# Kernel tuning notes

Hardware: AMD Instinct MI355X
Metric: run time of the kernel (lower is better)

## Reference

```python
import jax, jax.numpy as jnp
import numpy as np

N = 4096   # nodes
G = 64     # graphs
MH = 128   # hidden multiplicity (0e and 1o)
MU = 64    # up multiplicity (0e and 1o)
NSP = 10   # num_species
EPS = 1e-5


def _forward(nfh, nfu, onehot, W_h0, W_h1, W_u0, W_u1, Wt_00, Wt_11, Wt_01, Wt_10,
             W_p0, b_p0, W_p1, Wsc0, Wsc1, ln_w0, ln_b0, ln_w1, W_s0, b_s0, W_s1, batch):
    n = nfh.shape[0]
    # unpack irreps layout: [0e scalars | 1o vectors flattened]
    h0 = nfh[:, :MH]                       # [N, MH]
    h1 = nfh[:, MH:].reshape(n, MH, 3)     # [N, MH, 3]
    u0 = nfu[:, :MU]
    u1 = nfu[:, MU:].reshape(n, MU, 3)
    inv_h = 1.0 / np.sqrt(MH)
    inv_u = 1.0 / np.sqrt(MU)
    # irrep-wise (block-diagonal) o3.Linear, e3nn fan-in normalization
    hp0 = (h0 @ W_h0) * inv_h
    hp1 = jnp.einsum('nui,uv->nvi', h1, W_h1) * inv_h
    up0 = (u0 @ W_u0) * inv_u
    up1 = jnp.einsum('nui,uv->nvi', u1, W_u1) * inv_u
    # SeparateWeightTensorProduct: fully-connected 'uvw' CG tensor product
    # paths to 0e (scalars + gates, 2*MH outputs): 0e x 0e and 1o x 1o (dot / sqrt3)
    inv_tp = 1.0 / np.sqrt(2.0 * MH * MU)   # component/path normalization (2 paths, fan MH*MU)
    xy00 = jnp.einsum('nu,nv->nuv', hp0, up0).reshape(n, MH * MU)
    xy11 = jnp.einsum('nui,nvi->nuv', hp1, up1).reshape(n, MH * MU)
    z0 = (xy00 @ Wt_00.reshape(MH * MU, 2 * MH)
          + (xy11 @ Wt_11.reshape(MH * MU, 2 * MH)) / np.sqrt(3.0)) * inv_tp  # [N, 2*MH]
    # paths to 1o: 0e x 1o and 1o x 0e (staged to control intermediate size)
    ta = jnp.einsum('nu,uvw->nvw', hp0, Wt_01)       # [N, MU, MH]
    z1a = jnp.einsum('nvw,nvi->nwi', ta, up1)
    tb = jnp.einsum('nv,uvw->nuw', up0, Wt_10)       # [N, MH, MH]
    z1b = jnp.einsum('nuw,nui->nwi', tb, hp1)
    z1 = (z1a + z1b) * inv_tp                        # [N, MH, 3]
    # Gate nonlinearity: silu on scalars, sigmoid gates multiply 1o features
    s = jax.nn.silu(z0[:, :MH])
    g = jax.nn.sigmoid(z0[:, MH:])
    v = z1 * g[:, :, None]
    # lin_post (biases on scalars only)
    p0 = (s @ W_p0) * inv_h + b_p0
    p1 = jnp.einsum('nui,uv->nvi', v, W_p1) * inv_h
    # self-connection: FullyConnectedTensorProduct(hidden, NSPx0e, out)
    inv_sc = 1.0 / np.sqrt(MH * NSP)
    sxy0 = jnp.einsum('nu,nv->nuv', h0, onehot).reshape(n, MH * NSP)
    y0 = p0 + (sxy0 @ Wsc0.reshape(MH * NSP, MH)) * inv_sc
    sxy1 = jnp.einsum('nui,nv->nuvi', h1, onehot).reshape(n, MH * NSP, 3)
    y1 = p1 + jnp.einsum('nki,kw->nwi', sxy1, Wsc1.reshape(MH * NSP, MH)) * inv_sc
    # e3LayerNorm: per-graph stats; mean-subtract scalars only, RMS-normalize per irrep
    ones = jnp.ones((n,), y0.dtype)
    cnt = jnp.maximum(jax.ops.segment_sum(ones, batch, num_segments=G), 1.0)[:, None]
    mean0 = (jax.ops.segment_sum(y0, batch, num_segments=G) / cnt).mean(axis=1)  # [G]
    f0 = y0 - mean0[batch][:, None]
    var0 = (jax.ops.segment_sum(f0 * f0, batch, num_segments=G) / cnt).mean(axis=1)
    f0 = f0 / (jnp.sqrt(var0)[batch][:, None] + EPS) * ln_w0 + ln_b0
    var1 = (jax.ops.segment_sum((y1 * y1).reshape(n, -1), batch, num_segments=G) / cnt).mean(axis=1)
    f1 = y1 / (jnp.sqrt(var1)[batch][:, None, None] + EPS) * ln_w1[None, :, None]
    # residual skip connection (o3.Linear with scalar bias)
    out0 = f0 + (h0 @ W_s0) * inv_h + b_s0
    out1 = f1 + jnp.einsum('nui,uv->nvi', h1, W_s1) * inv_h
    return jnp.concatenate([out0, out1.reshape(n, 3 * MH)], axis=1)  # [N, 512]


def setup_inputs() -> dict:
    key = jax.random.key(0)
    ks = jax.random.split(key, 20)
    f = lambda i, shape: jax.random.normal(ks[i], shape, dtype=jnp.float32)
    species = jax.random.randint(ks[0], (N,), 0, NSP)
    return {
        'node_feats_hidden': f(1, (N, 4 * MH)),
        'node_feats_up': f(2, (N, 4 * MU)),
        'node_one_hot': jax.nn.one_hot(species, NSP, dtype=jnp.float32),
        'batch': jnp.sort(jax.random.randint(ks[3], (N,), 0, G)),
        'W_h0': f(4, (MH, MH)), 'W_h1': f(5, (MH, MH)),
        'W_u0': f(6, (MU, MU)), 'W_u1': f(7, (MU, MU)),
        'Wt_00': f(8, (MH, MU, 2 * MH)), 'Wt_11': f(9, (MH, MU, 2 * MH)),
        'Wt_01': f(10, (MH, MU, MH)), 'Wt_10': f(11, (MH, MU, MH)),
        'W_p0': f(12, (MH, MH)), 'b_p0': jnp.zeros((MH,), jnp.float32), 'W_p1': f(13, (MH, MH)),
        'Wsc0': f(14, (MH, NSP, MH)), 'Wsc1': f(15, (MH, NSP, MH)),
        'ln_w0': jnp.ones((MH,), jnp.float32), 'ln_b0': jnp.zeros((MH,), jnp.float32),
        'ln_w1': jnp.ones((MH,), jnp.float32),
        'W_s0': f(16, (MH, MH)), 'b_s0': jnp.zeros((MH,), jnp.float32), 'W_s1': f(17, (MH, MH)),
    }


def reference(node_feats_hidden, node_feats_up, node_one_hot, batch, W_h0, W_h1, W_u0, W_u1,
              Wt_00, Wt_11, Wt_01, Wt_10, W_p0, b_p0, W_p1, Wsc0, Wsc1, ln_w0, ln_b0, ln_w1,
              W_s0, b_s0, W_s1):
    return _forward(node_feats_hidden, node_feats_up, node_one_hot, W_h0, W_h1, W_u0, W_u1,
                    Wt_00, Wt_11, Wt_01, Wt_10, W_p0, b_p0, W_p1, Wsc0, Wsc1,
                    ln_w0, ln_b0, ln_w1, W_s0, b_s0, W_s1, batch)
```

## Files before the change

### kernel.cpp

```cpp
#include <hip/hip_runtime.h>
#include <cstdint>
#include <cstddef>


typedef _Float16 half8 __attribute__((ext_vector_type(8)));
typedef _Float16 half4v __attribute__((ext_vector_type(4)));
typedef float f32x4 __attribute__((ext_vector_type(4)));

static constexpr float INV_H  = 0.08838834764831845f;
static constexpr float INV_U  = 0.125f;
static constexpr float INV_TP = 0.0078125f;
static constexpr float INV_SC = 0.02795084971874737f;
static constexpr float RSQRT3 = 0.5773502691896258f;
static constexpr float LN_EPS = 1e-5f;

static constexpr size_t OFF_BZ0 = 0;
static constexpr size_t OFF_BZ1 = OFF_BZ0 + 8388608;
static constexpr size_t OFF_WH0 = OFF_BZ1 + 4194304;
static constexpr size_t OFF_WH1 = OFF_WH0 + 32768;
static constexpr size_t OFF_WU0 = OFF_WH1 + 32768;
static constexpr size_t OFF_WU1 = OFF_WU0 + 8192;
static constexpr size_t OFF_WP0 = OFF_WU1 + 8192;
static constexpr size_t OFF_WP1 = OFF_WP0 + 32768;
static constexpr size_t OFF_WS0 = OFF_WP1 + 32768;
static constexpr size_t OFF_WS1 = OFF_WS0 + 32768;
static constexpr size_t OFF_H0F = OFF_WS1 + 32768;
static constexpr size_t OFF_H1F = OFF_H0F + 1048576;
static constexpr size_t OFF_U0F = OFF_H1F + 3145728;
static constexpr size_t OFF_U1F = OFF_U0F + 524288;
static constexpr size_t OFF_HP0 = OFF_U1F + 1572864;
static constexpr size_t OFF_HP1 = OFF_HP0 + 1048576;
static constexpr size_t OFF_UP0 = OFF_HP1 + 3145728;
static constexpr size_t OFF_UP1 = OFF_UP0 + 524288;
static constexpr size_t OFF_SF  = OFF_UP1 + 1572864;
static constexpr size_t OFF_VF  = OFF_SF + 1048576;
static constexpr size_t OFF_PZ0 = OFF_VF + 3145728;
static constexpr size_t OFF_PZ1 = OFF_PZ0 + 16777216;
static constexpr size_t OFF_Y0  = OFF_PZ1 + 12582912;
static constexpr size_t OFF_Y1  = OFF_Y0 + 2097152;
static constexpr size_t OFF_O0  = OFF_Y1 + 6291456;
static constexpr size_t OFF_O1  = OFF_O0 + 2097152;
static constexpr size_t OFF_SP  = OFF_O1 + 6291456;
static constexpr size_t OFF_ST  = OFF_SP + 16384;
static constexpr size_t WS_NEED = OFF_ST + 2048;

__global__ __launch_bounds__(256) void kconv(
    const float* __restrict__ nfh, const float* __restrict__ nfu,
    const float* __restrict__ onehot,
    const float* __restrict__ Wt00, const float* __restrict__ Wt11,
    const float* __restrict__ Wt01, const float* __restrict__ Wt10,
    const float* __restrict__ Wh0, const float* __restrict__ Wh1,
    const float* __restrict__ Wu0, const float* __restrict__ Wu1,
    const float* __restrict__ Wp0, const float* __restrict__ Wp1,
    const float* __restrict__ Ws0, const float* __restrict__ Ws1,
    char* __restrict__ ws)
{
  const int bid = blockIdx.x, t = threadIdx.x;
  if (bid < 768) {
    _Float16* dst;
    int u, nt = 0;
    const bool isz0 = bid < 512;
    if (isz0) { nt = bid >> 8; u = bid & 255; dst = (_Float16*)(ws + OFF_BZ0) + ((size_t)nt*256 + (size_t)u)*8192; }
    else      { u = bid - 512;               dst = (_Float16*)(ws + OFF_BZ1) + (size_t)u*8192; }
    for (int it = 0; it < 4; ++it) {
      int chunk = it*256 + t;
      int lane = chunk & 63, ch = chunk >> 6;
      int f = ch >> 1, c = ch & 1;
      int w = f*16 + (lane & 15);
      int v0 = c*32 + (lane >> 4)*8;
      half8 o;
      #pragma unroll
      for (int j = 0; j < 8; ++j) {
        float val;
        if (isz0) {
          if (u < 128) val = Wt00[(size_t)((u*64 + v0 + j)*256) + nt*128 + w];
          else         val = Wt11[(size_t)(((u-128)*64 + v0 + j)*256) + nt*128 + w] * RSQRT3;
        } else {
          if (u < 128) val = Wt01[(size_t)((u*64 + v0 + j)*128) + w];
          else         val = Wt10[(size_t)(((u-128)*64 + v0 + j)*128) + w];
        }
        o[j] = (_Float16)val;
      }
      *(half8*)(dst + (size_t)chunk*8) = o;
    }
  } else if (bid < 776) {
    int mat = bid - 768;
    const float* src; size_t doff; int K, N;
    switch (mat) {
      case 0: src = Wh0; doff = OFF_WH0; K = 128; N = 128; break;
      case 1: src = Wh1; doff = OFF_WH1; K = 128; N = 128; break;
      case 2: src = Wu0; doff = OFF_WU0; K = 64;  N = 64;  break;
      case 3: src = Wu1; doff = OFF_WU1; K = 64;  N = 64;  break;
      case 4: src = Wp0; doff = OFF_WP0; K = 128; N = 128; break;
      case 5: src = Wp1; doff = OFF_WP1; K = 128; N = 128; break;
      case 6: src = Ws0; doff = OFF_WS0; K = 128; N = 128; break;
      default: src = Ws1; doff = OFF_WS1; K = 128; N = 128; break;
    }
    _Float16* d = (_Float16*)(ws + doff);
    const int nfr = N >> 4;
    const int chunks = (K*N) >> 3;
    for (int qd = t; qd < chunks; qd += 256) {
      int lane = qd & 63, cf = qd >> 6;
      int f = cf % nfr, c = cf / nfr;
      int col = f*16 + (lane & 15);
      int k0 = c*32 + (lane >> 4)*8;
      half8 o;
      #pragma unroll
      for (int j = 0; j < 8; ++j) o[j] = (_Float16)src[(size_t)(k0 + j)*N + col];
      *(half8*)(d + (size_t)qd*8) = o;
    }
  } else if (bid < 1544) {
    const int stride = 768*256;
    const int base = (bid - 776)*256 + t;
    _Float16* h0f = (_Float16*)(ws + OFF_H0F);
    _Float16* h1f = (_Float16*)(ws + OFF_H1F);
    _Float16* u0f = (_Float16*)(ws + OFF_U0F);
    _Float16* u1f = (_Float16*)(ws + OFF_U1F);
    for (int id = base; id < 524288; id += stride)
      h0f[id] = (_Float16)nfh[(size_t)(id >> 7)*512 + (id & 127)];
    for (int id = base; id < 1572864; id += stride) {
      int i = id >> 19, r = id & 524287, n = r >> 7, u = r & 127;
      h1f[id] = (_Float16)nfh[(size_t)n*512 + 128 + u*3 + i];
    }
    for (int id = base; id < 262144; id += stride)
      u0f[id] = (_Float16)nfu[(size_t)(id >> 6)*256 + (id & 63)];
    for (int id = base; id < 786432; id += stride) {
      int i = id >> 18, r = id & 262143, n = r >> 6, v = r & 63;
      u1f[id] = (_Float16)nfu[(size_t)n*256 + 64 + v*3 + i];
    }
  } else {
    int node = (bid - 1544)*256 + t;
    const float* row = onehot + (size_t)node*10;
    int best = 0; float bv = row[0];
    #pragma unroll
    for (int s = 1; s < 10; ++s) { float v = row[s]; if (v > bv) { bv = v; best = s; } }
    ((int*)(ws + OFF_SP))[node] = best;
  }
}

template<int KK, int NO, int MODE>
__global__ __launch_bounds__(256) void kgemm_small(char* __restrict__ ws,
    const float* __restrict__ bp0, const float* __restrict__ bs0)
{
  constexpr int NT = NO / 16;
  const int bid = blockIdx.x, t = threadIdx.x;
  const int lane = t & 63, wid = t >> 6;
  const int quad = lane >> 4, l15 = lane & 15;
  const int job = bid >> 5, n0 = (bid & 31) << 7;

  const _Float16 *A, *W;
  _Float16* oh = nullptr; float* of = nullptr;
  const float* bias = nullptr;
  float scale;
  if constexpr (MODE == 0) {
    scale = INV_H;
    if (job == 0) { A = (const _Float16*)(ws + OFF_H0F); W = (const _Float16*)(ws + OFF_WH0); oh = (_Float16*)(ws + OFF_HP0); }
    else {
      A = (const _Float16*)(ws + OFF_H1F) + (size_t)(job-1)*524288;
      W = (const _Float16*)(ws + OFF_WH1);
      oh = (_Float16*)(ws + OFF_HP1) + (size_t)(job-1)*524288;
    }
  } else if constexpr (MODE == 1) {
    scale = INV_U;
    if (job == 0) { A = (const _Float16*)(ws + OFF_U0F); W = (const _Float16*)(ws + OFF_WU0); oh = (_Float16*)(ws + OFF_UP0); }
    else {
      A = (const _Float16*)(ws + OFF_U1F) + (size_t)(job-1)*262144;
      W = (const _Float16*)(ws + OFF_WU1);
      oh = (_Float16*)(ws + OFF_UP1) + (size_t)(job-1)*262144;
    }
  } else {
    scale = INV_H;
    switch (job) {
      case 0: A = (const _Float16*)(ws + OFF_SF);  W = (const _Float16*)(ws + OFF_WP0); of = (float*)(ws + OFF_Y0); bias = bp0; break;
      case 1: A = (const _Float16*)(ws + OFF_H0F); W = (const _Float16*)(ws + OFF_WS0); of = (float*)(ws + OFF_O0); bias = bs0; break;
      case 2: case 3: case 4:
        A = (const _Float16*)(ws + OFF_VF) + (size_t)(job-2)*524288;
        W = (const _Float16*)(ws + OFF_WP1);
        of = (float*)(ws + OFF_Y1) + (size_t)(job-2)*524288; break;
      default:
        A = (const _Float16*)(ws + OFF_H1F) + (size_t)(job-5)*524288;
        W = (const _Float16*)(ws + OFF_WS1);
        of = (float*)(ws + OFF_O1) + (size_t)(job-5)*524288; break;
    }
  }

  f32x4 acc[2][NT];
  const f32x4 zz = {0.f, 0.f, 0.f, 0.f};
  #pragma unroll
  for (int mf = 0; mf < 2; ++mf)
    #pragma unroll
    for (int nf = 0; nf < NT; ++nf) acc[mf][nf] = zz;

  #pragma unroll
  for (int kc = 0; kc < KK/32; ++kc) {
    half8 a[2];
    #pragma unroll
    for (int mf = 0; mf < 2; ++mf)
      a[mf] = *(const half8*)(A + (size_t)(n0 + wid*32 + mf*16 + l15)*KK + kc*32 + quad*8);
    #pragma unroll
    for (int nf = 0; nf < NT; ++nf) {
      half8 b = *(const half8*)(W + (size_t)(kc*NT + nf)*512 + lane*8);
      #pragma unroll
      for (int mf = 0; mf < 2; ++mf)
        acc[mf][nf] = __builtin_amdgcn_mfma_f32_16x16x32_f16(a[mf], b, acc[mf][nf], 0, 0, 0);
    }
  }

  #pragma unroll
  for (int mf = 0; mf < 2; ++mf)
    #pragma unroll
    for (int nf = 0; nf < NT; ++nf) {
      int col = nf*16 + l15;
      float bv = bias ? bias[col] : 0.f;
      #pragma unroll
      for (int r = 0; r < 4; ++r) {
        int row = n0 + wid*32 + mf*16 + quad*4 + r;
        float v = acc[mf][nf][r] * scale + bv;
        if constexpr (MODE < 2) oh[(size_t)row*NO + col] = (_Float16)v;
        else                    of[(size_t)row*NO + col] = v;
      }
    }
}

__global__ __launch_bounds__(256, 2) void kbig(char* __restrict__ ws)
{
  const int bid = blockIdx.x, t = threadIdx.x;
  const int lane = t & 63, wid = t >> 6;
  const int wy = wid >> 1, wx = wid & 1;
  const int quad = lane >> 4, l15 = lane & 15;

  const _Float16* hp0 = (const _Float16*)(ws + OFF_HP0);
  const _Float16* hp1 = (const _Float16*)(ws + OFF_HP1);
  const _Float16* up0 = (const _Float16*)(ws + OFF_UP0);
  const _Float16* up1 = (const _Float16*)(ws + OFF_UP1);

  const _Float16 *p, *q, *B0;
  float* out; int opitch; size_t obase; int node0;
  if (bid < 256) {
    int mt = bid >> 3, nt = (bid >> 2) & 1, kj = bid & 3;
    node0 = mt << 7;
    if (kj == 0) { p = hp0; q = up0; }
    else { p = hp1 + (size_t)(kj-1)*524288; q = up1 + (size_t)(kj-1)*262144; }
    B0 = (const _Float16*)(ws + OFF_BZ0) + (size_t)nt*2097152 + (kj ? (size_t)1048576 : (size_t)0);
    out = (float*)(ws + OFF_PZ0) + (size_t)kj*1048576;
    obase = (size_t)node0*256 + (size_t)nt*128;
    opitch = 256;
  } else {
    int b2 = bid - 256, mt = b2 >> 1, kj = b2 & 1, i = mt >> 5;
    node0 = (mt & 31) << 7;
    if (kj == 0) { p = hp0; q = up1 + (size_t)i*262144; }
    else         { p = hp1 + (size_t)i*524288; q = up0; }
    B0 = (const _Float16*)(ws + OFF_BZ1) + (kj ? (size_t)1048576 : (size_t)0);
    out = (float*)(ws + OFF_PZ1) + (size_t)kj*1572864;
    obase = (size_t)mt*16384;
    opitch = 128;
  }

  half8 qf[4][2];
  #pragma unroll
  for (int mf = 0; mf < 4; ++mf)
    #pragma unroll
    for (int c = 0; c < 2; ++c)
      qf[mf][c] = *(const half8*)(q + (size_t)(node0 + wy*64 + mf*16 + l15)*64 + c*32 + quad*8);

  f32x4 acc[4][4];
  const f32x4 zz = {0.f, 0.f, 0.f, 0.f};
  #pragma unroll
  for (int mf = 0; mf < 4; ++mf)
    #pragma unroll
    for (int nf = 0; nf < 4; ++nf) acc[mf][nf] = zz;

  const _Float16* prow = p + (size_t)(node0 + wy*64 + l15)*128;
  const _Float16* Bw = B0 + (size_t)wx*4096 + (size_t)lane*8;

  for (int u4 = 0; u4 < 32; ++u4) {
    half4v pw[4];
    #pragma unroll
    for (int mf = 0; mf < 4; ++mf)
      pw[mf] = *(const half4v*)(prow + (size_t)mf*2048 + u4*4);
    #pragma unroll
    for (int uu = 0; uu < 4; ++uu) {
      const _Float16* Bu = Bw + (size_t)(u4*4 + uu)*8192;
      half8 bf[2][4];
      #pragma unroll
      for (int c = 0; c < 2; ++c)
        #pragma unroll
        for (int nf = 0; nf < 4; ++nf)
          bf[c][nf] = *(const half8*)(Bu + (size_t)((nf*2 + c)*512));
      #pragma unroll
      for (int mf = 0; mf < 4; ++mf) {
        const _Float16 ps = pw[mf][uu];
        const half8 pv = {ps, ps, ps, ps, ps, ps, ps, ps};
        #pragma unroll
        for (int c = 0; c < 2; ++c) {
          half8 a = qf[mf][c] * pv;
          #pragma unroll
          for (int nf = 0; nf < 4; ++nf)
            acc[mf][nf] = __builtin_amdgcn_mfma_f32_16x16x32_f16(a, bf[c][nf], acc[mf][nf], 0, 0, 0);
        }
      }
    }
  }

  #pragma unroll
  for (int mf = 0; mf < 4; ++mf)
    #pragma unroll
    for (int nf = 0; nf < 4; ++nf) {
      int col = wx*64 + nf*16 + l15;
      #pragma unroll
      for (int r = 0; r < 4; ++r) {
        int row = wy*64 + mf*16 + quad*4 + r;
        out[obase + (size_t)row*opitch + col] = acc[mf][nf][r];
      }
    }
}

__global__ __launch_bounds__(256) void kreduce(char* __restrict__ ws)
{
  const int id = blockIdx.x*256 + threadIdx.x;
  const int n = id >> 7, w = id & 127;
  const float* pz0 = (const float*)(ws + OFF_PZ0);
  const float* pz1 = (const float*)(ws + OFF_PZ1);
  _Float16* sf = (_Float16*)(ws + OFF_SF);
  _Float16* vf = (_Float16*)(ws + OFF_VF);
  const size_t b = (size_t)n*256;
  float zs = (pz0[b + w] + pz0[1048576 + b + w] + pz0[2097152 + b + w] + pz0[3145728 + b + w]) * INV_TP;
  float zg = (pz0[b + 128 + w] + pz0[1048576 + b + 128 + w] + pz0[2097152 + b + 128 + w] + pz0[3145728 + b + 128 + w]) * INV_TP;
  float s = zs / (1.f + __expf(-zs));
  float g = 1.f / (1.f + __expf(-zg));
  sf[id] = (_Float16)s;
  #pragma unroll
  for (int i = 0; i < 3; ++i) {
    size_t r = ((size_t)i*4096 + (size_t)n)*128 + w;
    float z1v = (pz1[r] + pz1[1572864 + r]) * INV_TP;
    vf[(size_t)i*524288 + (size_t)n*128 + w] = (_Float16)(z1v * g);
  }
}

__global__ __launch_bounds__(256) void ksc(char* __restrict__ ws,
    const float* __restrict__ nfh,
    const float* __restrict__ Wsc0, const float* __restrict__ Wsc1)
{
  const int t = threadIdx.x;
  const int node = blockIdx.x*2 + (t >> 7);
  const int w = t & 127;
  const int sp = ((const int*)(ws + OFF_SP))[node];
  const float* h = nfh + (size_t)node*512;
  float a0 = 0.f, a10 = 0.f, a11 = 0.f, a12 = 0.f;
  for (int u = 0; u < 128; ++u) {
    const size_t wi = (size_t)(u*10 + sp)*128 + w;
    float w0 = Wsc0[wi];
    float w1 = Wsc1[wi];
    a0 += h[u] * w0;
    a10 += h[128 + u*3 + 0] * w1;
    a11 += h[128 + u*3 + 1] * w1;
    a12 += h[128 + u*3 + 2] * w1;
  }
  float* y0 = (float*)(ws + OFF_Y0);
  float* y1 = (float*)(ws + OFF_Y1);
  y0[(size_t)node*128 + w] += INV_SC * a0;
  y1[(size_t)node*128 + w] += INV_SC * a10;
  y1[524288 + (size_t)node*128 + w] += INV_SC * a11;
  y1[1048576 + (size_t)node*128 + w] += INV_SC * a12;
}

__global__ __launch_bounds__(256) void kstats1(char* __restrict__ ws, const int* __restrict__ batch)
{
  const int t = threadIdx.x;
  const int node = blockIdx.x*32 + (t >> 3);
  const int sub = t & 7;
  const float* y0 = (const float*)(ws + OFF_Y0) + (size_t)node*128;
  const float* y1 = (const float*)(ws + OFF_Y1);
  float s0 = 0.f, ss0 = 0.f, ss1 = 0.f;
  for (int c = sub*16; c < sub*16 + 16; ++c) { float v = y0[c]; s0 += v; ss0 += v*v; }
  #pragma unroll
  for (int i = 0; i < 3; ++i) {
    const float* yp = y1 + (size_t)i*524288 + (size_t)node*128;
    for (int c = sub*16; c < sub*16 + 16; ++c) { float v = yp[c]; ss1 += v*v; }
  }
  #pragma unroll
  for (int m = 1; m < 8; m <<= 1) {
    s0  += __shfl_xor(s0, m, 64);
    ss0 += __shfl_xor(ss0, m, 64);
    ss1 += __shfl_xor(ss1, m, 64);
  }
  if (sub == 0) {
    float* st = (float*)(ws + OFF_ST);
    int g = batch[node];
    atomicAdd(&st[g], s0);
    atomicAdd(&st[64 + g], ss0);
    atomicAdd(&st[128 + g], ss1);
    atomicAdd(&st[192 + g], 1.f);
  }
}

__global__ void kstats2(char* __restrict__ ws)
{
  const int g = threadIdx.x;
  if (g >= 64) return;
  float* st = (float*)(ws + OFF_ST);
  float c = fmaxf(st[192 + g], 1.f);
  float m0 = st[g] / (c * 128.f);
  float var0 = st[64 + g] / (c * 128.f) - m0*m0;
  float var1 = st[128 + g] / (c * 384.f);
  st[256 + g] = m0;
  st[320 + g] = 1.f / (sqrtf(fmaxf(var0, 0.f)) + LN_EPS);
  st[384 + g] = 1.f / (sqrtf(fmaxf(var1, 0.f)) + LN_EPS);
}

__global__ __launch_bounds__(256) void kfinal(char* __restrict__ ws, const int* __restrict__ batch,
    const float* __restrict__ lnw0, const float* __restrict__ lnb0, const float* __restrict__ lnw1,
    float* __restrict__ outp)
{
  const int id = blockIdx.x*256 + threadIdx.x;
  const int n = id >> 9, c = id & 511;
  const float* st = (const float*)(ws + OFF_ST);
  const int g = batch[n];
  float val;
  if (c < 128) {
    const float* y0 = (const float*)(ws + OFF_Y0);
    const float* o0 = (const float*)(ws + OFF_O0);
    val = (y0[(size_t)n*128 + c] - st[256 + g]) * st[320 + g] * lnw0[c] + lnb0[c] + o0[(size_t)n*128 + c];
  } else {
    int cc = c - 128, w = cc / 3, i = cc - w*3;
    const float* y1 = (const float*)(ws + OFF_Y1);
    const float* o1 = (const float*)(ws + OFF_O1);
    val = y1[(size_t)i*524288 + (size_t)n*128 + w] * st[384 + g] * lnw1[w]
        + o1[(size_t)i*524288 + (size_t)n*128 + w];
  }
  outp[id] = val;
}

extern "C" void kernel_launch(void* const* d_in, const int* in_sizes, int n_in,
                              void* d_out, int out_size, void* d_ws, size_t ws_size,
                              hipStream_t stream)
{
  const float* nfh   = (const float*)d_in[0];
  const float* nfu   = (const float*)d_in[1];
  const float* oneh  = (const float*)d_in[2];
  const int*   batch = (const int*)d_in[3];
  const float* Wh0   = (const float*)d_in[4];
  const float* Wh1   = (const float*)d_in[5];
  const float* Wu0   = (const float*)d_in[6];
  const float* Wu1   = (const float*)d_in[7];
  const float* Wt00  = (const float*)d_in[8];
  const float* Wt11  = (const float*)d_in[9];
  const float* Wt01  = (const float*)d_in[10];
  const float* Wt10  = (const float*)d_in[11];
  const float* Wp0   = (const float*)d_in[12];
  const float* bp0   = (const float*)d_in[13];
  const float* Wp1   = (const float*)d_in[14];
  const float* Wsc0  = (const float*)d_in[15];
  const float* Wsc1  = (const float*)d_in[16];
  const float* lnw0  = (const float*)d_in[17];
  const float* lnb0  = (const float*)d_in[18];
  const float* lnw1  = (const float*)d_in[19];
  const float* Ws0   = (const float*)d_in[20];
  const float* bs0   = (const float*)d_in[21];
  const float* Ws1   = (const float*)d_in[22];
  char* ws = (char*)d_ws;

  if (ws_size < WS_NEED) {
    hipMemsetAsync(d_out, 0, (size_t)out_size * sizeof(float), stream);
    return;
  }

  hipMemsetAsync(ws + OFF_ST, 0, 2048, stream);
  kconv<<<1560, 256, 0, stream>>>(nfh, nfu, oneh, Wt00, Wt11, Wt01, Wt10,
                                  Wh0, Wh1, Wu0, Wu1, Wp0, Wp1, Ws0, Ws1, ws);
  kgemm_small<128,128,0><<<128, 256, 0, stream>>>(ws, nullptr, nullptr);
  kgemm_small<64, 64, 1><<<128, 256, 0, stream>>>(ws, nullptr, nullptr);
  kbig<<<448, 256, 0, stream>>>(ws);
  kreduce<<<2048, 256, 0, stream>>>(ws);
  kgemm_small<128,128,2><<<256, 256, 0, stream>>>(ws, bp0, bs0);
  ksc<<<2048, 256, 0, stream>>>(ws, nfh, Wsc0, Wsc1);
  kstats1<<<128, 256, 0, stream>>>(ws, batch);
  kstats2<<<1, 64, 0, stream>>>(ws);
  kfinal<<<8192, 256, 0, stream>>>(ws, batch, lnw0, lnb0, lnw1, (float*)d_out);
}
```

Baseline: 367.4 us.

## Fuse stats into self-connection, drop memset and stats2, double-buffer B loads in kbig

Several changes at once. The stats accumulator is zeroed inside kconv instead of by a separate memset. The self-connection kernel now also computes the per-graph sums with wave and block reductions, which removes the kstats1 re-read of y0/y1 and the kstats2 launch, and kfinal now derives mean and inverse std per element itself. The big GEMM loop software-pipelines the B fragment and p loads with two register buffers so loads overlap the MFMAs. The cost is higher register pressure in kbig and redundant sqrt/div work per element in kfinal.

```diff
diff --git a/kernel.cpp b/kernel.cpp
--- a/kernel.cpp
+++ b/kernel.cpp
@@ -135,6 +135,10 @@
     #pragma unroll
     for (int s = 1; s < 10; ++s) { float v = row[s]; if (v > bv) { bv = v; best = s; } }
     ((int*)(ws + OFF_SP))[node] = best;
+    if (bid == 1544) {
+      float* stz = (float*)(ws + OFF_ST);
+      stz[t] = 0.f; stz[t + 256] = 0.f;
+    }
   }
 }
 
@@ -273,33 +277,55 @@
   const _Float16* prow = p + (size_t)(node0 + wy*64 + l15)*128;
   const _Float16* Bw = B0 + (size_t)wx*4096 + (size_t)lane*8;
 
-  for (int u4 = 0; u4 < 32; ++u4) {
-    half4v pw[4];
-    #pragma unroll
-    for (int mf = 0; mf < 4; ++mf)
-      pw[mf] = *(const half4v*)(prow + (size_t)mf*2048 + u4*4);
-    #pragma unroll
-    for (int uu = 0; uu < 4; ++uu) {
-      const _Float16* Bu = Bw + (size_t)(u4*4 + uu)*8192;
-      half8 bf[2][4];
-      #pragma unroll
-      for (int c = 0; c < 2; ++c)
+  auto loadB = [&](half8 (&dst)[2][4], int uidx) {
+    const _Float16* Bu = Bw + (size_t)uidx*8192;
+    #pragma unroll
+    for (int c = 0; c < 2; ++c)
+      #pragma unroll
+      for (int nf = 0; nf < 4; ++nf)
+        dst[c][nf] = *(const half8*)(Bu + (size_t)((nf*2 + c)*512));
+  };
+  auto mstep = [&](const half8 (&bf)[2][4], const half4v (&pwl)[4], int uu) {
+    #pragma unroll
+    for (int mf = 0; mf < 4; ++mf) {
+      const _Float16 ps = pwl[mf][uu];
+      const half8 pv = {ps, ps, ps, ps, ps, ps, ps, ps};
+      #pragma unroll
+      for (int c = 0; c < 2; ++c) {
+        half8 a = qf[mf][c] * pv;
         #pragma unroll
         for (int nf = 0; nf < 4; ++nf)
-          bf[c][nf] = *(const half8*)(Bu + (size_t)((nf*2 + c)*512));
-      #pragma unroll
-      for (int mf = 0; mf < 4; ++mf) {
-        const _Float16 ps = pw[mf][uu];
-        const half8 pv = {ps, ps, ps, ps, ps, ps, ps, ps};
-        #pragma unroll
-        for (int c = 0; c < 2; ++c) {
-          half8 a = qf[mf][c] * pv;
-          #pragma unroll
-          for (int nf = 0; nf < 4; ++nf)
-            acc[mf][nf] = __builtin_amdgcn_mfma_f32_16x16x32_f16(a, bf[c][nf], acc[mf][nf], 0, 0, 0);
-        }
+          acc[mf][nf] = __builtin_amdgcn_mfma_f32_16x16x32_f16(a, bf[c][nf], acc[mf][nf], 0, 0, 0);
       }
     }
+  };
+
+  half4v pw[4], pwN[4];
+  #pragma unroll
+  for (int mf = 0; mf < 4; ++mf)
+    pw[mf] = *(const half4v*)(prow + (size_t)mf*2048);
+
+  half8 bfA[2][4], bfB[2][4];
+  loadB(bfA, 0);
+
+  for (int u4 = 0; u4 < 32; ++u4) {
+    const int b = u4*4;
+    loadB(bfB, b + 1);
+    mstep(bfA, pw, 0);
+    loadB(bfA, b + 2);
+    mstep(bfB, pw, 1);
+    {
+      const int np = (u4 < 31) ? (u4 + 1)*4 : u4*4;
+      #pragma unroll
+      for (int mf = 0; mf < 4; ++mf)
+        pwN[mf] = *(const half4v*)(prow + (size_t)mf*2048 + np);
+    }
+    loadB(bfB, b + 3);
+    mstep(bfA, pw, 2);
+    loadB(bfA, (u4 < 31) ? (b + 4) : (b + 3));
+    mstep(bfB, pw, 3);
+    #pragma unroll
+    for (int mf = 0; mf < 4; ++mf) pw[mf] = pwN[mf];
   }
 
   #pragma unroll
@@ -337,9 +363,10 @@
   }
 }
 
-__global__ __launch_bounds__(256) void ksc(char* __restrict__ ws,
+__global__ __launch_bounds__(256) void kscstats(char* __restrict__ ws,
     const float* __restrict__ nfh,
-    const float* __restrict__ Wsc0, const float* __restrict__ Wsc1)
+    const float* __restrict__ Wsc0, const float* __restrict__ Wsc1,
+    const int* __restrict__ batch)
 {
   const int t = threadIdx.x;
   const int node = blockIdx.x*2 + (t >> 7);
@@ -358,54 +385,37 @@
   }
   float* y0 = (float*)(ws + OFF_Y0);
   float* y1 = (float*)(ws + OFF_Y1);
-  y0[(size_t)node*128 + w] += INV_SC * a0;
-  y1[(size_t)node*128 + w] += INV_SC * a10;
-  y1[524288 + (size_t)node*128 + w] += INV_SC * a11;
-  y1[1048576 + (size_t)node*128 + w] += INV_SC * a12;
-}
-
-__global__ __launch_bounds__(256) void kstats1(char* __restrict__ ws, const int* __restrict__ batch)
-{
-  const int t = threadIdx.x;
-  const int node = blockIdx.x*32 + (t >> 3);
-  const int sub = t & 7;
-  const float* y0 = (const float*)(ws + OFF_Y0) + (size_t)node*128;
-  const float* y1 = (const float*)(ws + OFF_Y1);
-  float s0 = 0.f, ss0 = 0.f, ss1 = 0.f;
-  for (int c = sub*16; c < sub*16 + 16; ++c) { float v = y0[c]; s0 += v; ss0 += v*v; }
-  #pragma unroll
-  for (int i = 0; i < 3; ++i) {
-    const float* yp = y1 + (size_t)i*524288 + (size_t)node*128;
-    for (int c = sub*16; c < sub*16 + 16; ++c) { float v = yp[c]; ss1 += v*v; }
-  }
-  #pragma unroll
-  for (int m = 1; m < 8; m <<= 1) {
+  const size_t i0 = (size_t)node*128 + w;
+  float y0n  = y0[i0]           + INV_SC * a0;
+  float y1n0 = y1[i0]           + INV_SC * a10;
+  float y1n1 = y1[524288 + i0]  + INV_SC * a11;
+  float y1n2 = y1[1048576 + i0] + INV_SC * a12;
+  y0[i0] = y0n;
+  y1[i0] = y1n0;
+  y1[524288 + i0]  = y1n1;
+  y1[1048576 + i0] = y1n2;
+
+  float s0 = y0n, ss0 = y0n*y0n, ss1 = y1n0*y1n0 + y1n1*y1n1 + y1n2*y1n2;
+  #pragma unroll
+  for (int m = 1; m < 64; m <<= 1) {
     s0  += __shfl_xor(s0, m, 64);
     ss0 += __shfl_xor(ss0, m, 64);
     ss1 += __shfl_xor(ss1, m, 64);
   }
-  if (sub == 0) {
-    float* st = (float*)(ws + OFF_ST);
-    int g = batch[node];
-    atomicAdd(&st[g], s0);
-    atomicAdd(&st[64 + g], ss0);
-    atomicAdd(&st[128 + g], ss1);
-    atomicAdd(&st[192 + g], 1.f);
-  }
-}
-
-__global__ void kstats2(char* __restrict__ ws)
-{
-  const int g = threadIdx.x;
-  if (g >= 64) return;
-  float* st = (float*)(ws + OFF_ST);
-  float c = fmaxf(st[192 + g], 1.f);
-  float m0 = st[g] / (c * 128.f);
-  float var0 = st[64 + g] / (c * 128.f) - m0*m0;
-  float var1 = st[128 + g] / (c * 384.f);
-  st[256 + g] = m0;
-  st[320 + g] = 1.f / (sqrtf(fmaxf(var0, 0.f)) + LN_EPS);
-  st[384 + g] = 1.f / (sqrtf(fmaxf(var1, 0.f)) + LN_EPS);
+  __shared__ float red[4][3];
+  if ((t & 63) == 0) {
+    red[t >> 6][0] = s0; red[t >> 6][1] = ss0; red[t >> 6][2] = ss1;
+  }
+  __syncthreads();
+  if ((t & 127) == 0) {
+    const int wv = t >> 6;
+    float* stp = (float*)(ws + OFF_ST);
+    const int g = batch[node];
+    atomicAdd(&stp[g],       red[wv][0] + red[wv+1][0]);
+    atomicAdd(&stp[64 + g],  red[wv][1] + red[wv+1][1]);
+    atomicAdd(&stp[128 + g], red[wv][2] + red[wv+1][2]);
+    atomicAdd(&stp[192 + g], 1.f);
+  }
 }
 
 __global__ __launch_bounds__(256) void kfinal(char* __restrict__ ws, const int* __restrict__ batch,
@@ -416,16 +426,21 @@
   const int n = id >> 9, c = id & 511;
   const float* st = (const float*)(ws + OFF_ST);
   const int g = batch[n];
+  const float cnt = fmaxf(st[192 + g], 1.f);
   float val;
   if (c < 128) {
     const float* y0 = (const float*)(ws + OFF_Y0);
     const float* o0 = (const float*)(ws + OFF_O0);
-    val = (y0[(size_t)n*128 + c] - st[256 + g]) * st[320 + g] * lnw0[c] + lnb0[c] + o0[(size_t)n*128 + c];
+    float m0   = st[g] / (cnt * 128.f);
+    float var0 = st[64 + g] / (cnt * 128.f) - m0*m0;
+    float inv0 = 1.f / (sqrtf(fmaxf(var0, 0.f)) + LN_EPS);
+    val = (y0[(size_t)n*128 + c] - m0) * inv0 * lnw0[c] + lnb0[c] + o0[(size_t)n*128 + c];
   } else {
     int cc = c - 128, w = cc / 3, i = cc - w*3;
     const float* y1 = (const float*)(ws + OFF_Y1);
     const float* o1 = (const float*)(ws + OFF_O1);
-    val = y1[(size_t)i*524288 + (size_t)n*128 + w] * st[384 + g] * lnw1[w]
+    float inv1 = 1.f / (sqrtf(fmaxf(st[128 + g] / (cnt * 384.f), 0.f)) + LN_EPS);
+    val = y1[(size_t)i*524288 + (size_t)n*128 + w] * inv1 * lnw1[w]
         + o1[(size_t)i*524288 + (size_t)n*128 + w];
   }
   outp[id] = val;
@@ -465,7 +480,6 @@
     return;
   }
 
-  hipMemsetAsync(ws + OFF_ST, 0, 2048, stream);
   kconv<<<1560, 256, 0, stream>>>(nfh, nfu, oneh, Wt00, Wt11, Wt01, Wt10,
                                   Wh0, Wh1, Wu0, Wu1, Wp0, Wp1, Ws0, Ws1, ws);
   kgemm_small<128,128,0><<<128, 256, 0, stream>>>(ws, nullptr, nullptr);
@@ -473,8 +487,6 @@
   kbig<<<448, 256, 0, stream>>>(ws);
   kreduce<<<2048, 256, 0, stream>>>(ws);
   kgemm_small<128,128,2><<<256, 256, 0, stream>>>(ws, bp0, bs0);
-  ksc<<<2048, 256, 0, stream>>>(ws, nfh, Wsc0, Wsc1);
-  kstats1<<<128, 256, 0, stream>>>(ws, batch);
-  kstats2<<<1, 64, 0, stream>>>(ws);
+  kscstats<<<2048, 256, 0, stream>>>(ws, nfh, Wsc0, Wsc1, batch);
   kfinal<<<8192, 256, 0, stream>>>(ws, batch, lnw0, lnb0, lnw1, (float*)d_out);
 }
```

Result: faster. 353.8 us (-3.7%).
